# Optimization experiments

Measured on AMD Instinct MI355X. Metric: run time of the kernel, lower is better.

Reference implementation:

```python
import jax, jax.numpy as jnp
import numpy as np

B, S, D = 4, 2048, 1024
H, Dh = 16, 64


def setup_inputs() -> dict:
    key = jax.random.key(0)
    ks = jax.random.split(key, 9)
    s_in = 1.0 / np.sqrt(D)
    inp = {
        "key": jax.random.normal(ks[0], (B, S, D), jnp.float32),
        "value": jax.random.normal(ks[1], (B, S, D), jnp.float32),
        "query": jax.random.normal(ks[2], (B, S, D), jnp.float32),
        # Linear weights stored as [in, out] (math-equivalent to torch W.T)
        "Wq": jax.random.uniform(ks[3], (D, H * Dh), jnp.float32, -s_in, s_in),
        "bq": jax.random.uniform(ks[4], (H * Dh,), jnp.float32, -s_in, s_in),
        "Wk": jax.random.uniform(ks[5], (D, H * Dh), jnp.float32, -s_in, s_in),
        "bk": jax.random.uniform(ks[6], (H * Dh,), jnp.float32, -s_in, s_in),
        "Wv": jax.random.uniform(ks[7], (D, H * Dh), jnp.float32, -s_in, s_in),
        "bv": jax.random.uniform(ks[8], (H * Dh,), jnp.float32, -s_in, s_in),
    }
    return inp


def reference(key, value, query, Wq, bq, Wk, bk, Wv, bv):
    b, s, _ = key.shape
    # projections -> [B, H, S, Dh]
    q = (query @ Wq + bq).reshape(b, s, H, Dh).transpose(0, 2, 1, 3)
    k = (key @ Wk + bk).reshape(b, s, H, Dh).transpose(0, 2, 1, 3)
    v = (value @ Wv + bv).reshape(b, s, H, Dh).transpose(0, 2, 1, 3)
    scores = jnp.einsum("bhqd,bhkd->bhqk", q, k) / np.sqrt(Dh).astype(np.float32)
    p = jax.nn.softmax(scores, axis=-1)
    out = jnp.einsum("bhqk,bhkd->bhqd", p, v)  # [B, H, S, Dh]
    return out.transpose(0, 2, 1, 3).reshape(b, s, H * Dh)
```

## Files before the change

### kernel.cpp

```cpp
#include <hip/hip_runtime.h>

typedef __bf16 bf16;
typedef __bf16 bf16x8 __attribute__((ext_vector_type(8)));
typedef __bf16 bf16x4 __attribute__((ext_vector_type(4)));
typedef _Float16 f16x4 __attribute__((ext_vector_type(4)));
typedef _Float16 f16x8 __attribute__((ext_vector_type(8)));
typedef __fp16 h16x2 __attribute__((ext_vector_type(2)));
typedef float  f32x4  __attribute__((ext_vector_type(4)));
typedef float  f32x16 __attribute__((ext_vector_type(16)));
typedef unsigned int uint2v __attribute__((ext_vector_type(2)));
typedef unsigned int uint4v __attribute__((ext_vector_type(4)));

#define LOG2E 1.44269504088896340736f
#define SCQ (0.125f * LOG2E)

__device__ __forceinline__ void async16(const void* g, void* l) {
  __builtin_amdgcn_global_load_lds(
      (const __attribute__((address_space(1))) unsigned int*)g,
      (__attribute__((address_space(3))) unsigned int*)l, 16, 0, 0);
}

__device__ __forceinline__ f32x4 mfma_bf16(bf16x8 a, bf16x8 b, f32x4 c) {
  return __builtin_amdgcn_mfma_f32_16x16x32_bf16(a, b, c, 0, 0, 0);
}
__device__ __forceinline__ f32x16 mfma32_bf16(bf16x8 a, bf16x8 b, f32x16 c) {
  return __builtin_amdgcn_mfma_f32_32x32x16_bf16(a, b, c, 0, 0, 0);
}
__device__ __forceinline__ f32x16 mfma32x16_f16(f16x8 a, f16x8 b, f32x16 c) {
  return __builtin_amdgcn_mfma_f32_32x32x16_f16(a, b, c, 0, 0, 0);
}

__global__ __launch_bounds__(256) void prep(const float* __restrict__ q,
                                            const float* __restrict__ k,
                                            const float* __restrict__ v,
                                            const float* __restrict__ W0,
                                            const float* __restrict__ W1,
                                            const float* __restrict__ W2,
                                            bf16* __restrict__ actb,
                                            bf16* __restrict__ Wt) {
  __shared__ float t[64 * 69];
  const int z = blockIdx.y, tid = threadIdx.x;
  if (blockIdx.x < 4096) {
    const float* in = z == 0 ? q : (z == 1 ? k : v);
    bf16* o = actb + (size_t)z * 8388608;
    int i = blockIdx.x * 256 + tid;
    const float4* p = (const float4*)in;
    float4 a = p[i * 2], c = p[i * 2 + 1];
    bf16x8 r;
    r[0] = (bf16)a.x; r[1] = (bf16)a.y; r[2] = (bf16)a.z; r[3] = (bf16)a.w;
    r[4] = (bf16)c.x; r[5] = (bf16)c.y; r[6] = (bf16)c.z; r[7] = (bf16)c.w;
    ((bf16x8*)o)[i] = r;
  } else {
    const float* W = z == 0 ? W0 : (z == 1 ? W1 : W2);
    bf16* O = Wt + (size_t)z * (1024 * 1024);
    int lin = blockIdx.x - 4096;
    int k0 = (lin & 15) * 64, n0 = (lin >> 4) * 64;
    int r0 = tid >> 4, c0 = (tid & 15) * 4;
#pragma unroll
    for (int rr = 0; rr < 4; rr++) {
      int kk = r0 + rr * 16;
      float4 vv = *(const float4*)(W + (k0 + kk) * 1024 + n0 + c0);
      t[kk * 69 + c0 + 0] = vv.x; t[kk * 69 + c0 + 1] = vv.y;
      t[kk * 69 + c0 + 2] = vv.z; t[kk * 69 + c0 + 3] = vv.w;
    }
    __syncthreads();
#pragma unroll
    for (int rr = 0; rr < 4; rr++) {
      int n = r0 + rr * 16;
      bf16x4 o;
#pragma unroll
      for (int j = 0; j < 4; j++) o[j] = (bf16)t[(c0 + j) * 69 + n];
      *(bf16x4*)(O + (n0 + n) * 1024 + k0 + c0) = o;
    }
  }
}

__global__ __launch_bounds__(256, 3) void gemm_qkv(const bf16* __restrict__ Act,
                                                   const bf16* __restrict__ Wt,
                                                   const float* __restrict__ b0,
                                                   const float* __restrict__ b1,
                                                   const float* __restrict__ b2,
                                                   bf16* __restrict__ qo,
                                                   bf16* __restrict__ ko,
                                                   _Float16* __restrict__ vf) {
  __shared__ bf16 smem[16384];
  bf16* sA = smem;
  bf16* sB = smem + 8192;
  const int tid = threadIdx.x;
  const int wave = tid >> 6, lane = tid & 63;
  const int quad = lane >> 4, l15 = lane & 15;
  const int z = blockIdx.z;
  const int m0 = blockIdx.x * 128, n0 = blockIdx.y * 128;
  const bf16* A = Act + (size_t)z * 8388608;
  const bf16* Bt = Wt + (size_t)z * 1048576;
  const float* bias = z == 0 ? b0 : (z == 1 ? b1 : b2);

  const bf16* ap[4]; const bf16* bp[4]; int lo[4];
#pragma unroll
  for (int i = 0; i < 4; i++) {
    int g = wave * 256 + i * 64 + lane;
    int row = g >> 3, jl = (g & 7) ^ (row & 7);
    ap[i] = A + (m0 + row) * 1024 + jl * 8;
    bp[i] = Bt + (n0 + row) * 1024 + jl * 8;
    lo[i] = (wave * 256 + i * 64) * 8;
  }
  const int wm = (wave & 1) * 64, wn = (wave >> 1) * 64;
  f32x4 acc[4][4] = {};

  for (int kt = 0; kt < 16; kt++) {
    const int ko_ = kt * 64;
#pragma unroll
    for (int i = 0; i < 4; i++) async16(ap[i] + ko_, sA + lo[i]);
#pragma unroll
    for (int i = 0; i < 4; i++) async16(bp[i] + ko_, sB + lo[i]);
    __syncthreads();
#pragma unroll
    for (int ks = 0; ks < 2; ks++) {
      bf16x8 af[4], bv[4];
#pragma unroll
      for (int mt = 0; mt < 4; mt++) {
        int m = wm + mt * 16 + l15;
        int ph = (ks * 4 + quad) ^ (m & 7);
        af[mt] = *(const bf16x8*)(sA + m * 64 + ph * 8);
      }
#pragma unroll
      for (int nt = 0; nt < 4; nt++) {
        int n = wn + nt * 16 + l15;
        int ph = (ks * 4 + quad) ^ (n & 7);
        bv[nt] = *(const bf16x8*)(sB + n * 64 + ph * 8);
      }
#pragma unroll
      for (int mt = 0; mt < 4; mt++)
#pragma unroll
        for (int nt = 0; nt < 4; nt++)
          acc[mt][nt] = mfma_bf16(af[mt], bv[nt], acc[mt][nt]);
    }
    __syncthreads();
  }

  if (z != 2) {
    bf16* O = z == 0 ? qo : ko;
    const float sc = z == 0 ? SCQ : 1.0f;
#pragma unroll
    for (int nt = 0; nt < 4; nt++) {
      int n = n0 + wn + nt * 16 + l15;
      float bc = bias[n];
#pragma unroll
      for (int mt = 0; mt < 4; mt++)
#pragma unroll
        for (int r = 0; r < 4; r++) {
          int m = m0 + wm + mt * 16 + quad * 4 + r;
          O[m * 1024 + n] = (bf16)((acc[mt][nt][r] + bc) * sc);
        }
    }
  } else {
    const int b = m0 >> 11, s0 = m0 & 2047;
    const int kvb = s0 >> 7;
    const int mtg0 = (wave & 1) * 4;
    const int hl = quad >> 1, jb = (quad & 1) * 4;
#pragma unroll
    for (int nt = 0; nt < 4; nt++) {
      int n = n0 + wn + nt * 16;
      int hh = n >> 6, db = (n >> 5) & 1;
      int lanep = hl * 32 + (n & 31) + l15;
      float bc = bias[n + l15];
#pragma unroll
      for (int mt = 0; mt < 4; mt++) {
        int fi = (mtg0 + mt) * 2 + db;
        f16x4 pk;
#pragma unroll
        for (int r = 0; r < 4; r++) pk[r] = (_Float16)(acc[mt][nt][r] + bc);
        size_t off = ((((size_t)(b * 16 + hh) * 16 + kvb) * 16 + fi) * 512)
                     + lanep * 8 + jb;
        *(f16x4*)(vf + off) = pk;
      }
    }
  }
}

__global__ __launch_bounds__(256, 3) void attn(const bf16* __restrict__ Q,
                                               const bf16* __restrict__ K,
                                               const _Float16* __restrict__ VF,
                                               float* __restrict__ Out) {
  __shared__ bf16 sQ[8192];
  __shared__ bf16 sK0[4096], sK1[4096];
  __shared__ _Float16 sV0[4096], sV1[4096];
  const int tid = threadIdx.x;
  const int wave = tid >> 6, lane = tid & 63;
  const int l31 = lane & 31, hl = lane >> 5;
  const int q0 = blockIdx.x * 128, hh = blockIdx.y, b = blockIdx.z;
  const bf16* Kbase = K + (size_t)(b * 2048) * 1024 + hh * 64;
  const _Float16* Vbase = VF + (size_t)(b * 16 + hh) * 131072;

  const int g0 = tid, g1 = 256 + tid;
  const int r0s = g0 >> 3, j0s = (g0 & 7) ^ (r0s & 7);
  const int r1s = g1 >> 3, j1s = (g1 & 7) ^ (r1s & 7);
  const bf16* kst0 = Kbase + (size_t)r0s * 1024 + j0s * 8;
  const bf16* kst1 = Kbase + (size_t)r1s * 1024 + j1s * 8;

  auto stageKV = [&](int t, bf16* sk, _Float16* sv) {
    async16(kst0 + (size_t)t * 65536, sk + g0 * 8);
    async16(kst1 + (size_t)t * 65536, sk + g1 * 8);
    async16(Vbase + t * 4096 + g0 * 8, sv + g0 * 8);
    async16(Vbase + t * 4096 + g1 * 8, sv + g1 * 8);
  };

#pragma unroll
  for (int i = 0; i < 4; i++) {
    int g = i * 256 + tid;
    int row = g >> 3, jl = (g & 7) ^ (row & 7);
    async16(Q + (size_t)(b * 2048 + q0 + row) * 1024 + hh * 64 + jl * 8, sQ + g * 8);
  }
  stageKV(0, sK0, sV0);
  __syncthreads();

  bf16x8 qf[4];
  {
    int rowq = wave * 32 + l31, rx = rowq & 7;
#pragma unroll
    for (int i = 0; i < 4; i++)
      qf[i] = *(const bf16x8*)(sQ + rowq * 64 + ((2 * i + hl) ^ rx) * 8);
  }

  f32x16 oacc[2] = {};
  float ls = 0.f;

  auto computeT = [&](const bf16* sk, const _Float16* sv) {
#pragma unroll
    for (int t32 = 0; t32 < 2; t32++) {
      int rowk = t32 * 32 + l31, rx = rowk & 7;
      const bf16* kr = sk + rowk * 64;
      f32x16 st = {};
#pragma unroll
      for (int i = 0; i < 4; i++) {
        bf16x8 kf = *(const bf16x8*)(kr + ((2 * i + hl) ^ rx) * 8);
        st = mfma32_bf16(kf, qf[i], st);
      }
      unsigned int dw[8];
      float ps = 0.f;
#pragma unroll
      for (int s = 0; s < 4; s++) {
        float p0 = __builtin_amdgcn_exp2f(st[4 * s + 0]);
        float p1 = __builtin_amdgcn_exp2f(st[4 * s + 1]);
        float p2 = __builtin_amdgcn_exp2f(st[4 * s + 2]);
        float p3 = __builtin_amdgcn_exp2f(st[4 * s + 3]);
        ps += (p0 + p1) + (p2 + p3);
        dw[2 * s]     = __builtin_bit_cast(unsigned int,
                          __builtin_amdgcn_cvt_pkrtz(p0, p1));
        dw[2 * s + 1] = __builtin_bit_cast(unsigned int,
                          __builtin_amdgcn_cvt_pkrtz(p2, p3));
      }
      ls += ps;
#pragma unroll
      for (int u = 0; u < 2; u++) {
        uint2v rA = __builtin_amdgcn_permlane32_swap(dw[4 * u + 0],
                                                     dw[4 * u + 2], false, false);
        uint2v rB = __builtin_amdgcn_permlane32_swap(dw[4 * u + 1],
                                                     dw[4 * u + 3], false, false);
        uint4v uu;
        uu[0] = rA[0]; uu[1] = rB[0]; uu[2] = rA[1]; uu[3] = rB[1];
        f16x8 pfrag = __builtin_bit_cast(f16x8, uu);
#pragma unroll
        for (int db = 0; db < 2; db++) {
          f16x8 va = *(const f16x8*)(sv + ((t32 * 4 + u * 2 + db) * 64 + lane) * 8);
          oacc[db] = mfma32x16_f16(va, pfrag, oacc[db]);
        }
      }
    }
  };

#pragma unroll 1
  for (int t = 0; t < 32; t += 2) {
    stageKV(t + 1, sK1, sV1);
    computeT(sK0, sV0);
    __syncthreads();
    if (t + 2 < 32) stageKV(t + 2, sK0, sV0);
    computeT(sK1, sV1);
    __syncthreads();
  }

  ls += __shfl_xor(ls, 32);
  float inv = 1.f / ls;
  int qrow = b * 2048 + q0 + wave * 32 + l31;
  float* orow = Out + (size_t)qrow * 1024 + hh * 64;
#pragma unroll
  for (int db = 0; db < 2; db++)
#pragma unroll
    for (int rg = 0; rg < 4; rg++) {
      float4 v;
      v.x = oacc[db][4 * rg + 0] * inv;
      v.y = oacc[db][4 * rg + 1] * inv;
      v.z = oacc[db][4 * rg + 2] * inv;
      v.w = oacc[db][4 * rg + 3] * inv;
      *(float4*)(orow + db * 32 + rg * 8 + 4 * hl) = v;
    }
}

extern "C" void kernel_launch(void* const* d_in, const int* in_sizes, int n_in,
                              void* d_out, int out_size, void* d_ws, size_t ws_size,
                              hipStream_t stream) {
  const float* key   = (const float*)d_in[0];
  const float* value = (const float*)d_in[1];
  const float* query = (const float*)d_in[2];
  const float* Wq = (const float*)d_in[3];
  const float* bq = (const float*)d_in[4];
  const float* Wk = (const float*)d_in[5];
  const float* bk = (const float*)d_in[6];
  const float* Wv = (const float*)d_in[7];
  const float* bv = (const float*)d_in[8];
  float* out = (float*)d_out;

  char* ws = (char*)d_ws;
  bf16* actb   = (bf16*)(ws);
  bf16* wt     = (bf16*)(ws + 50331648);
  bf16* qo     = (bf16*)(ws + 56623104);
  bf16* ko     = (bf16*)(ws + 73400320);
  _Float16* vf = (_Float16*)(ws + 90177536);
  (void)in_sizes; (void)n_in; (void)out_size; (void)ws_size;

  prep<<<dim3(4352, 3), 256, 0, stream>>>(query, key, value, Wq, Wk, Wv, actb, wt);
  gemm_qkv<<<dim3(64, 8, 3), 256, 0, stream>>>(actb, wt, bq, bk, bv, qo, ko, vf);
  attn<<<dim3(16, 16, 4), 256, 0, stream>>>(qo, ko, vf, out);
}
```

Measured before the change: 290.0 us.

## Process two 32-row query chunks per wave to reuse K/V fragments

Each attention block now covers 256 query rows instead of 128, and each wave handles two 32-row query chunks. The K and V fragments read from LDS are shared by both chunks, which halves LDS traffic and the global K/V staging per query row. MFMA sections are wrapped in s_setprio to favour matrix issue. The cost is more registers (launch bounds drop from 3 to 2 waves per SIMD), more LDS for Q, and half as many blocks in the grid.

```diff
diff --git a/kernel.cpp b/kernel.cpp
--- a/kernel.cpp
+++ b/kernel.cpp
@@ -178,17 +178,17 @@
   }
 }
 
-__global__ __launch_bounds__(256, 3) void attn(const bf16* __restrict__ Q,
+__global__ __launch_bounds__(256, 2) void attn(const bf16* __restrict__ Q,
                                                const bf16* __restrict__ K,
                                                const _Float16* __restrict__ VF,
                                                float* __restrict__ Out) {
-  __shared__ bf16 sQ[8192];
+  __shared__ bf16 sQ[16384];
   __shared__ bf16 sK0[4096], sK1[4096];
   __shared__ _Float16 sV0[4096], sV1[4096];
   const int tid = threadIdx.x;
   const int wave = tid >> 6, lane = tid & 63;
   const int l31 = lane & 31, hl = lane >> 5;
-  const int q0 = blockIdx.x * 128, hh = blockIdx.y, b = blockIdx.z;
+  const int q0 = blockIdx.x * 256, hh = blockIdx.y, b = blockIdx.z;
   const bf16* Kbase = K + (size_t)(b * 2048) * 1024 + hh * 64;
   const _Float16* Vbase = VF + (size_t)(b * 16 + hh) * 131072;
 
@@ -206,7 +206,7 @@
   };
 
 #pragma unroll
-  for (int i = 0; i < 4; i++) {
+  for (int i = 0; i < 8; i++) {
     int g = i * 256 + tid;
     int row = g >> 3, jl = (g & 7) ^ (row & 7);
     async16(Q + (size_t)(b * 2048 + q0 + row) * 1024 + hh * 64 + jl * 8, sQ + g * 8);
@@ -214,58 +214,76 @@
   stageKV(0, sK0, sV0);
   __syncthreads();
 
-  bf16x8 qf[4];
-  {
-    int rowq = wave * 32 + l31, rx = rowq & 7;
+  bf16x8 qf[2][4];
+#pragma unroll
+  for (int qc = 0; qc < 2; qc++) {
+    int rowq = wave * 64 + qc * 32 + l31, rx = rowq & 7;
 #pragma unroll
     for (int i = 0; i < 4; i++)
-      qf[i] = *(const bf16x8*)(sQ + rowq * 64 + ((2 * i + hl) ^ rx) * 8);
-  }
-
-  f32x16 oacc[2] = {};
-  float ls = 0.f;
+      qf[qc][i] = *(const bf16x8*)(sQ + rowq * 64 + ((2 * i + hl) ^ rx) * 8);
+  }
+
+  f32x16 oacc0[2] = {}, oacc1[2] = {};
+  float ls0 = 0.f, ls1 = 0.f;
+
+  auto procP = [&](const f32x16& st, float& lsum, f32x16* oq, const f16x8* va) {
+    unsigned int dw[8];
+    float ps = 0.f;
+#pragma unroll
+    for (int s = 0; s < 4; s++) {
+      float p0 = __builtin_amdgcn_exp2f(st[4 * s + 0]);
+      float p1 = __builtin_amdgcn_exp2f(st[4 * s + 1]);
+      float p2 = __builtin_amdgcn_exp2f(st[4 * s + 2]);
+      float p3 = __builtin_amdgcn_exp2f(st[4 * s + 3]);
+      ps += (p0 + p1) + (p2 + p3);
+      dw[2 * s]     = __builtin_bit_cast(unsigned int,
+                        __builtin_amdgcn_cvt_pkrtz(p0, p1));
+      dw[2 * s + 1] = __builtin_bit_cast(unsigned int,
+                        __builtin_amdgcn_cvt_pkrtz(p2, p3));
+    }
+    lsum += ps;
+#pragma unroll
+    for (int u = 0; u < 2; u++) {
+      uint2v rA = __builtin_amdgcn_permlane32_swap(dw[4 * u + 0],
+                                                   dw[4 * u + 2], false, false);
+      uint2v rB = __builtin_amdgcn_permlane32_swap(dw[4 * u + 1],
+                                                   dw[4 * u + 3], false, false);
+      uint4v uu;
+      uu[0] = rA[0]; uu[1] = rB[0]; uu[2] = rA[1]; uu[3] = rB[1];
+      f16x8 pfrag = __builtin_bit_cast(f16x8, uu);
+      __builtin_amdgcn_s_setprio(1);
+#pragma unroll
+      for (int db = 0; db < 2; db++)
+        oq[db] = mfma32x16_f16(va[u * 2 + db], pfrag, oq[db]);
+      __builtin_amdgcn_s_setprio(0);
+    }
+  };
 
   auto computeT = [&](const bf16* sk, const _Float16* sv) {
 #pragma unroll
     for (int t32 = 0; t32 < 2; t32++) {
       int rowk = t32 * 32 + l31, rx = rowk & 7;
       const bf16* kr = sk + rowk * 64;
-      f32x16 st = {};
-#pragma unroll
-      for (int i = 0; i < 4; i++) {
-        bf16x8 kf = *(const bf16x8*)(kr + ((2 * i + hl) ^ rx) * 8);
-        st = mfma32_bf16(kf, qf[i], st);
-      }
-      unsigned int dw[8];
-      float ps = 0.f;
-#pragma unroll
-      for (int s = 0; s < 4; s++) {
-        float p0 = __builtin_amdgcn_exp2f(st[4 * s + 0]);
-        float p1 = __builtin_amdgcn_exp2f(st[4 * s + 1]);
-        float p2 = __builtin_amdgcn_exp2f(st[4 * s + 2]);
-        float p3 = __builtin_amdgcn_exp2f(st[4 * s + 3]);
-        ps += (p0 + p1) + (p2 + p3);
-        dw[2 * s]     = __builtin_bit_cast(unsigned int,
-                          __builtin_amdgcn_cvt_pkrtz(p0, p1));
-        dw[2 * s + 1] = __builtin_bit_cast(unsigned int,
-                          __builtin_amdgcn_cvt_pkrtz(p2, p3));
-      }
-      ls += ps;
-#pragma unroll
-      for (int u = 0; u < 2; u++) {
-        uint2v rA = __builtin_amdgcn_permlane32_swap(dw[4 * u + 0],
-                                                     dw[4 * u + 2], false, false);
-        uint2v rB = __builtin_amdgcn_permlane32_swap(dw[4 * u + 1],
-                                                     dw[4 * u + 3], false, false);
-        uint4v uu;
-        uu[0] = rA[0]; uu[1] = rB[0]; uu[2] = rA[1]; uu[3] = rB[1];
-        f16x8 pfrag = __builtin_bit_cast(f16x8, uu);
-#pragma unroll
-        for (int db = 0; db < 2; db++) {
-          f16x8 va = *(const f16x8*)(sv + ((t32 * 4 + u * 2 + db) * 64 + lane) * 8);
-          oacc[db] = mfma32x16_f16(va, pfrag, oacc[db]);
-        }
-      }
+      bf16x8 kf[4];
+#pragma unroll
+      for (int i = 0; i < 4; i++)
+        kf[i] = *(const bf16x8*)(kr + ((2 * i + hl) ^ rx) * 8);
+      f32x16 st0 = {}, st1 = {};
+      __builtin_amdgcn_s_setprio(1);
+#pragma unroll
+      for (int i = 0; i < 4; i++) st0 = mfma32_bf16(kf[i], qf[0][i], st0);
+#pragma unroll
+      for (int i = 0; i < 4; i++) st1 = mfma32_bf16(kf[i], qf[1][i], st1);
+      __builtin_amdgcn_s_setprio(0);
+      f16x8 va[4];
+#pragma unroll
+      for (int u = 0; u < 2; u++)
+#pragma unroll
+        for (int db = 0; db < 2; db++)
+          va[u * 2 + db] =
+              *(const f16x8*)(sv + ((t32 * 4 + u * 2 + db) * 64 + lane) * 8);
+      procP(st0, ls0, oacc0, va);
+      procP(st1, ls1, oacc1, va);
     }
   };
 
@@ -279,21 +297,26 @@
     __syncthreads();
   }
 
-  ls += __shfl_xor(ls, 32);
-  float inv = 1.f / ls;
-  int qrow = b * 2048 + q0 + wave * 32 + l31;
-  float* orow = Out + (size_t)qrow * 1024 + hh * 64;
-#pragma unroll
-  for (int db = 0; db < 2; db++)
-#pragma unroll
-    for (int rg = 0; rg < 4; rg++) {
-      float4 v;
-      v.x = oacc[db][4 * rg + 0] * inv;
-      v.y = oacc[db][4 * rg + 1] * inv;
-      v.z = oacc[db][4 * rg + 2] * inv;
-      v.w = oacc[db][4 * rg + 3] * inv;
-      *(float4*)(orow + db * 32 + rg * 8 + 4 * hl) = v;
-    }
+  ls0 += __shfl_xor(ls0, 32);
+  ls1 += __shfl_xor(ls1, 32);
+#pragma unroll
+  for (int qc = 0; qc < 2; qc++) {
+    float inv = 1.f / (qc == 0 ? ls0 : ls1);
+    const f32x16* oq = qc == 0 ? oacc0 : oacc1;
+    int qrow = b * 2048 + q0 + wave * 64 + qc * 32 + l31;
+    float* orow = Out + (size_t)qrow * 1024 + hh * 64;
+#pragma unroll
+    for (int db = 0; db < 2; db++)
+#pragma unroll
+      for (int rg = 0; rg < 4; rg++) {
+        float4 v;
+        v.x = oq[db][4 * rg + 0] * inv;
+        v.y = oq[db][4 * rg + 1] * inv;
+        v.z = oq[db][4 * rg + 2] * inv;
+        v.w = oq[db][4 * rg + 3] * inv;
+        *(float4*)(orow + db * 32 + rg * 8 + 4 * hl) = v;
+      }
+  }
 }
 
 extern "C" void kernel_launch(void* const* d_in, const int* in_sizes, int n_in,
@@ -320,5 +343,5 @@
 
   prep<<<dim3(4352, 3), 256, 0, stream>>>(query, key, value, Wq, Wk, Wv, actb, wt);
   gemm_qkv<<<dim3(64, 8, 3), 256, 0, stream>>>(actb, wt, bq, bk, bv, qo, ko, vf);
-  attn<<<dim3(16, 16, 4), 256, 0, stream>>>(qo, ko, vf, out);
-}
+  attn<<<dim3(8, 16, 4), 256, 0, stream>>>(qo, ko, vf, out);
+}
```

Result: no change. 289.7 us (-0.1%).
